# Optimization experiments

Measured on AMD Instinct MI355X. Metric: run time of the kernel, lower is better.

The kernel has to match this reference:

```python
import jax, jax.numpy as jnp
import numpy as np

VOCAB = 50257
D_MODEL = 1024
PAD_IDX = 0
B, L = 4, 4096


def setup_inputs() -> dict:
    key = jax.random.key(0)
    k1, k2, k3, k4, k5 = jax.random.split(key, 5)
    input_ids = jax.random.randint(k1, (B, L), 0, VOCAB, dtype=jnp.int64 if jax.config.jax_enable_x64 else jnp.int32)
    role_mask = jax.random.randint(k2, (B, L), 0, 2, dtype=input_ids.dtype)
    emb = jax.random.normal(k3, (VOCAB, D_MODEL), dtype=jnp.float32)
    emb = emb.at[PAD_IDX].set(0.0)  # padding_idx row is zero in nn.Embedding
    # nn.Linear weight has shape (out, in); y = x @ W.T
    scale = 1.0 / np.sqrt(D_MODEL)
    W0 = jax.random.uniform(k4, (D_MODEL, D_MODEL), dtype=jnp.float32, minval=-scale, maxval=scale)
    W1 = jax.random.uniform(k5, (D_MODEL, D_MODEL), dtype=jnp.float32, minval=-scale, maxval=scale)
    return {"input_ids": input_ids, "role_mask": role_mask, "emb": emb, "W0": W0, "W1": W1}


def reference(input_ids, role_mask, emb, W0, W1):
    # Embedding lookup: (B, L, D)
    x = emb[input_ids]
    # Per-role linear transform (2-expert routing); compute both, select by mask.
    y0 = jnp.einsum('bld,ed->ble', x, W0)
    y1 = jnp.einsum('bld,ed->ble', x, W1)
    out = jnp.where((role_mask == 1)[..., None], y1, y0)
    return out
```

## Files before the change

kernel.cpp:

```cpp
#include <hip/hip_runtime.h>


#define M_TOK   16384
#define DIM     1024
#define MT      128
#define NTIL    130
#define XROWS   (NTIL * MT)
#define BK      64
#define PBLK    64
#define WBLKS   2048

typedef __attribute__((ext_vector_type(8))) short short8;
typedef __attribute__((ext_vector_type(4))) float f32x4;

#define OFF_PERM 256
#define OFF_WB   66816
#define OFF_X    4261120

static __device__ __forceinline__ unsigned short f2bf(float f) {
    unsigned int u = __float_as_uint(f);
    u += 0x7fffu + ((u >> 16) & 1u);
    return (unsigned short)(u >> 16);
}

__global__ void k_pre(const int* __restrict__ role, int* perm, int* cnt,
                      const float* __restrict__ W0, const float* __restrict__ W1,
                      unsigned short* __restrict__ Wb) {
    int b = blockIdx.x;
    if (b < PBLK) {
        int t = b * 256 + threadIdx.x;
        int row;
        if (role[t] == 1) { int s = atomicAdd(&cnt[1], 1); row = XROWS - 1 - s; }
        else              { int s = atomicAdd(&cnt[0], 1); row = s; }
        perm[row] = t;
    } else {
        int idx = ((b - PBLK) * 256 + threadIdx.x) * 4;
        const float* src = (idx < 1048576) ? (W0 + idx) : (W1 + (idx - 1048576));
        float4 f = *(const float4*)src;
        *(ushort4*)(Wb + idx) = make_ushort4(f2bf(f.x), f2bf(f.y), f2bf(f.z), f2bf(f.w));
    }
}

__global__ void k_gather(const int* __restrict__ ids, const int* __restrict__ perm,
                         const int* __restrict__ cnt, const float* __restrict__ emb,
                         unsigned short* __restrict__ X) {
    int b = blockIdx.x;
    int n0 = cnt[0], n1 = cnt[1];
    if (b >= n0 && b < XROWS - n1) return;
    int p = perm[b];
    int id = ids[p];
    int t = threadIdx.x;
    float4 f = *(const float4*)(emb + (size_t)id * DIM + t * 4);
    *(ushort4*)(X + (size_t)b * DIM + t * 4) =
        make_ushort4(f2bf(f.x), f2bf(f.y), f2bf(f.z), f2bf(f.w));
}

__global__ __launch_bounds__(256, 3)
void k_gemm(const unsigned short* __restrict__ Xu, const unsigned short* __restrict__ Wbu,
            const int* __restrict__ perm, const int* __restrict__ cnt,
            float* __restrict__ out) {
    __shared__ short As[MT * BK];
    __shared__ short Bs[MT * BK];

    int f  = blockIdx.x;
    int mt = ((f >> 6) << 3) | (f & 7);
    int nt = (f >> 3) & 7;
    if (mt >= NTIL) return;

    int n0 = cnt[0], n1 = cnt[1];
    int T0 = (n0 + 127) >> 7, T1 = (n1 + 127) >> 7;
    int e, lo, hi;
    if (mt < T0)              { e = 0; lo = 0;            hi = n0;    }
    else if (mt >= NTIL - T1) { e = 1; lo = XROWS - n1;   hi = XROWS; }
    else return;

    const short* Ag = (const short*)Xu + (size_t)mt * MT * DIM;
    const short* Bg = (const short*)Wbu + (size_t)e * DIM * DIM + (size_t)nt * MT * DIM;

    int tid  = threadIdx.x;
    int lane = tid & 63;
    int w    = tid >> 6;
    int wm   = w & 1, wn = w >> 1;
    int quad = lane >> 4, lq = lane & 15;

    f32x4 acc[4][4] = {};

    for (int k0 = 0; k0 < DIM; k0 += BK) {
#pragma unroll
        for (int i = 0; i < 4; ++i) {
            int q   = w * 4 + i;
            int s   = q * 64 + lane;
            int row = s >> 3;
            int kc  = (s & 7) ^ (row & 7);
            __builtin_amdgcn_global_load_lds(
                (const __attribute__((address_space(1))) unsigned int*)(Ag + (size_t)row * DIM + k0 + kc * 8),
                (__attribute__((address_space(3))) unsigned int*)(&As[s * 8]),
                16, 0, 0);
            __builtin_amdgcn_global_load_lds(
                (const __attribute__((address_space(1))) unsigned int*)(Bg + (size_t)row * DIM + k0 + kc * 8),
                (__attribute__((address_space(3))) unsigned int*)(&Bs[s * 8]),
                16, 0, 0);
        }
        __syncthreads();

#pragma unroll
        for (int s = 0; s < 2; ++s) {
            short8 av[4], bv[4];
            int s4q = s * 4 + quad;
#pragma unroll
            for (int i = 0; i < 4; ++i) {
                int ra = wm * 64 + i * 16 + lq;
                av[i] = *(const short8*)&As[(ra * 8 + (s4q ^ (ra & 7))) * 8];
                int rb = wn * 64 + i * 16 + lq;
                bv[i] = *(const short8*)&Bs[(rb * 8 + (s4q ^ (rb & 7))) * 8];
            }
#pragma unroll
            for (int i = 0; i < 4; ++i)
#pragma unroll
                for (int j = 0; j < 4; ++j)
                    acc[i][j] = __builtin_amdgcn_mfma_f32_16x16x32_bf16(
                        av[i], bv[j], acc[i][j], 0, 0, 0);
        }
        __syncthreads();
    }

    int colbase = nt * 128 + wn * 64 + lq;
#pragma unroll
    for (int i = 0; i < 4; ++i) {
#pragma unroll
        for (int r = 0; r < 4; ++r) {
            int mrow = mt * MT + wm * 64 + i * 16 + quad * 4 + r;
            if (mrow < lo || mrow >= hi) continue;
            int token = perm[mrow];
            float* o = out + (size_t)token * DIM + colbase;
#pragma unroll
            for (int j = 0; j < 4; ++j)
                o[j * 16] = acc[i][j][r];
        }
    }
}

extern "C" void kernel_launch(void* const* d_in, const int* in_sizes, int n_in,
                              void* d_out, int out_size, void* d_ws, size_t ws_size,
                              hipStream_t stream) {
    const int*   ids  = (const int*)d_in[0];
    const int*   role = (const int*)d_in[1];
    const float* emb  = (const float*)d_in[2];
    const float* W0   = (const float*)d_in[3];
    const float* W1   = (const float*)d_in[4];
    float*       out  = (float*)d_out;

    char* ws = (char*)d_ws;
    int* cnt  = (int*)ws;
    int* perm = (int*)(ws + OFF_PERM);
    unsigned short* Wb = (unsigned short*)(ws + OFF_WB);
    unsigned short* X  = (unsigned short*)(ws + OFF_X);

    hipMemsetAsync(cnt, 0x00, 2 * sizeof(int), stream);
    k_pre   <<<PBLK + WBLKS, 256, 0, stream>>>(role, perm, cnt, W0, W1, Wb);
    k_gather<<<XROWS,        256, 0, stream>>>(ids, perm, cnt, emb, X);
    k_gemm  <<<1088,         256, 0, stream>>>(X, Wb, perm, cnt, out);
}
```

Before: 326.3 us.

## Fuse embedding gather into GEMM by loading fp32 rows directly to LDS

Removes the separate gather kernel that wrote a bf16 copy of the gathered embeddings. The GEMM now loads fp32 embedding rows straight into shared memory through per-row token ids and converts them to bf16 in registers before the MFMA. The token-id table is filled in the prep kernel and padding rows default to id 0 via the memset. This saves one launch and a round trip through an intermediate buffer. In exchange the A tile doubles in LDS size and global traffic, which may lower occupancy, and every block redoes the conversion.

```diff
diff --git a/kernel.cpp b/kernel.cpp
--- a/kernel.cpp
+++ b/kernel.cpp
@@ -1,4 +1,5 @@
 #include <hip/hip_runtime.h>
+#include <hip/hip_bf16.h>
 
 
 #define M_TOK   16384
@@ -12,10 +13,11 @@
 
 typedef __attribute__((ext_vector_type(8))) short short8;
 typedef __attribute__((ext_vector_type(4))) float f32x4;
+typedef __attribute__((ext_vector_type(4))) unsigned int uint32x4;
 
-#define OFF_PERM 256
-#define OFF_WB   66816
-#define OFF_X    4261120
+#define OFF_TOK  256
+#define OFF_PERM 66816
+#define OFF_WB   133376
 
 static __device__ __forceinline__ unsigned short f2bf(float f) {
     unsigned int u = __float_as_uint(f);
@@ -23,7 +25,15 @@
     return (unsigned short)(u >> 16);
 }
 
-__global__ void k_pre(const int* __restrict__ role, int* perm, int* cnt,
+static __device__ __forceinline__ unsigned int pk2(float a, float b) {
+    __hip_bfloat162 h = __float22bfloat162_rn(make_float2(a, b));
+    union { __hip_bfloat162 h; unsigned int u; } c;
+    c.h = h;
+    return c.u;
+}
+
+__global__ void k_pre(const int* __restrict__ role, const int* __restrict__ ids,
+                      int* perm, int* tokid, int* cnt,
                       const float* __restrict__ W0, const float* __restrict__ W1,
                       unsigned short* __restrict__ Wb) {
     int b = blockIdx.x;
@@ -32,7 +42,8 @@
         int row;
         if (role[t] == 1) { int s = atomicAdd(&cnt[1], 1); row = XROWS - 1 - s; }
         else              { int s = atomicAdd(&cnt[0], 1); row = s; }
-        perm[row] = t;
+        perm[row]  = t;
+        tokid[row] = ids[t];
     } else {
         int idx = ((b - PBLK) * 256 + threadIdx.x) * 4;
         const float* src = (idx < 1048576) ? (W0 + idx) : (W1 + (idx - 1048576));
@@ -41,25 +52,11 @@
     }
 }
 
-__global__ void k_gather(const int* __restrict__ ids, const int* __restrict__ perm,
-                         const int* __restrict__ cnt, const float* __restrict__ emb,
-                         unsigned short* __restrict__ X) {
-    int b = blockIdx.x;
-    int n0 = cnt[0], n1 = cnt[1];
-    if (b >= n0 && b < XROWS - n1) return;
-    int p = perm[b];
-    int id = ids[p];
-    int t = threadIdx.x;
-    float4 f = *(const float4*)(emb + (size_t)id * DIM + t * 4);
-    *(ushort4*)(X + (size_t)b * DIM + t * 4) =
-        make_ushort4(f2bf(f.x), f2bf(f.y), f2bf(f.z), f2bf(f.w));
-}
-
 __global__ __launch_bounds__(256, 3)
-void k_gemm(const unsigned short* __restrict__ Xu, const unsigned short* __restrict__ Wbu,
-            const int* __restrict__ perm, const int* __restrict__ cnt,
-            float* __restrict__ out) {
-    __shared__ short As[MT * BK];
+void k_gemm(const float* __restrict__ emb, const unsigned short* __restrict__ Wbu,
+            const int* __restrict__ perm, const int* __restrict__ tokid,
+            const int* __restrict__ cnt, float* __restrict__ out) {
+    __shared__ float As[MT * BK];
     __shared__ short Bs[MT * BK];
 
     int f  = blockIdx.x;
@@ -74,7 +71,6 @@
     else if (mt >= NTIL - T1) { e = 1; lo = XROWS - n1;   hi = XROWS; }
     else return;
 
-    const short* Ag = (const short*)Xu + (size_t)mt * MT * DIM;
     const short* Bg = (const short*)Wbu + (size_t)e * DIM * DIM + (size_t)nt * MT * DIM;
 
     int tid  = threadIdx.x;
@@ -83,21 +79,38 @@
     int wm   = w & 1, wn = w >> 1;
     int quad = lane >> 4, lq = lane & 15;
 
+    unsigned int aoff[8];
+#pragma unroll
+    for (int q = 0; q < 8; ++q) {
+        int row = 16 * q + 4 * w + quad;
+        int kf  = (((lq >> 1) ^ (row & 7)) << 3) | ((lq & 1) << 2);
+        aoff[q] = (unsigned int)tokid[mt * MT + row] * (DIM * 4) + kf * 4;
+    }
+    unsigned int boff[4];
+#pragma unroll
+    for (int q = 0; q < 4; ++q) {
+        int s   = (q * 4 + w) * 64 + lane;
+        int row = s >> 3;
+        int kc  = (s & 7) ^ (row & 7);
+        boff[q] = (unsigned int)(row * DIM + kc * 8) * 2;
+    }
+
     f32x4 acc[4][4] = {};
 
     for (int k0 = 0; k0 < DIM; k0 += BK) {
 #pragma unroll
-        for (int i = 0; i < 4; ++i) {
-            int q   = w * 4 + i;
-            int s   = q * 64 + lane;
-            int row = s >> 3;
-            int kc  = (s & 7) ^ (row & 7);
+        for (int q = 0; q < 8; ++q) {
+            int s = (q * 4 + w) * 64 + lane;
             __builtin_amdgcn_global_load_lds(
-                (const __attribute__((address_space(1))) unsigned int*)(Ag + (size_t)row * DIM + k0 + kc * 8),
-                (__attribute__((address_space(3))) unsigned int*)(&As[s * 8]),
+                (const __attribute__((address_space(1))) unsigned int*)((const char*)emb + aoff[q] + k0 * 4),
+                (__attribute__((address_space(3))) unsigned int*)(&As[s * 4]),
                 16, 0, 0);
+        }
+#pragma unroll
+        for (int q = 0; q < 4; ++q) {
+            int s = (q * 4 + w) * 64 + lane;
             __builtin_amdgcn_global_load_lds(
-                (const __attribute__((address_space(1))) unsigned int*)(Bg + (size_t)row * DIM + k0 + kc * 8),
+                (const __attribute__((address_space(1))) unsigned int*)((const char*)Bg + boff[q] + k0 * 2),
                 (__attribute__((address_space(3))) unsigned int*)(&Bs[s * 8]),
                 16, 0, 0);
         }
@@ -105,21 +118,29 @@
 
 #pragma unroll
         for (int s = 0; s < 2; ++s) {
-            short8 av[4], bv[4];
             int s4q = s * 4 + quad;
+            short8 bv[4];
+#pragma unroll
+            for (int j = 0; j < 4; ++j) {
+                int rb = wn * 64 + j * 16 + lq;
+                bv[j] = *(const short8*)&Bs[(rb * 8 + (s4q ^ (rb & 7))) * 8];
+            }
 #pragma unroll
             for (int i = 0; i < 4; ++i) {
                 int ra = wm * 64 + i * 16 + lq;
-                av[i] = *(const short8*)&As[(ra * 8 + (s4q ^ (ra & 7))) * 8];
-                int rb = wn * 64 + i * 16 + lq;
-                bv[i] = *(const short8*)&Bs[(rb * 8 + (s4q ^ (rb & 7))) * 8];
-            }
-#pragma unroll
-            for (int i = 0; i < 4; ++i)
+                int p  = s4q ^ (ra & 7);
+                const f32x4* ap = (const f32x4*)&As[ra * BK + p * 8];
+                f32x4 fl = ap[0], fh = ap[1];
+                union { uint32x4 u; short8 v; } av;
+                av.u[0] = pk2(fl[0], fl[1]);
+                av.u[1] = pk2(fl[2], fl[3]);
+                av.u[2] = pk2(fh[0], fh[1]);
+                av.u[3] = pk2(fh[2], fh[3]);
 #pragma unroll
                 for (int j = 0; j < 4; ++j)
                     acc[i][j] = __builtin_amdgcn_mfma_f32_16x16x32_bf16(
-                        av[i], bv[j], acc[i][j], 0, 0, 0);
+                        av.v, bv[j], acc[i][j], 0, 0, 0);
+            }
         }
         __syncthreads();
     }
@@ -151,13 +172,12 @@
     float*       out  = (float*)d_out;
 
     char* ws = (char*)d_ws;
-    int* cnt  = (int*)ws;
-    int* perm = (int*)(ws + OFF_PERM);
+    int* cnt   = (int*)ws;
+    int* tokid = (int*)(ws + OFF_TOK);
+    int* perm  = (int*)(ws + OFF_PERM);
     unsigned short* Wb = (unsigned short*)(ws + OFF_WB);
-    unsigned short* X  = (unsigned short*)(ws + OFF_X);
 
-    hipMemsetAsync(cnt, 0x00, 2 * sizeof(int), stream);
-    k_pre   <<<PBLK + WBLKS, 256, 0, stream>>>(role, perm, cnt, W0, W1, Wb);
-    k_gather<<<XROWS,        256, 0, stream>>>(ids, perm, cnt, emb, X);
-    k_gemm  <<<1088,         256, 0, stream>>>(X, Wb, perm, cnt, out);
+    hipMemsetAsync(ws, 0x00, OFF_PERM, stream);
+    k_pre <<<PBLK + WBLKS, 256, 0, stream>>>(role, ids, perm, tokid, cnt, W0, W1, Wb);
+    k_gemm<<<1088,         256, 0, stream>>>(emb, Wb, perm, tokid, cnt, out);
 }
```

After: 345.6 us. 1.06x slower.
